# Optimization experiments

Hardware: AMD Instinct MI355X
Metric: run time of the kernel (lower is better)

## Reference

```python
import jax, jax.numpy as jnp
from jax import lax
import numpy as np

B, C, H, W = 32, 64, 80, 80


def setup_inputs() -> dict:
    key = jax.random.key(0)
    ks = jax.random.split(key, 9)
    x = jax.random.normal(ks[0], (B, C, H, W), dtype=jnp.float32)
    # gammas are zero-init Parameters in torch; use small random values so the
    # recurrence is non-trivial but numerically stable (spectral radius ~0.4).
    g = lambda k: jax.random.normal(k, (C, C), dtype=jnp.float32) * 0.05
    return {"x": x,
            "g1": g(ks[1]), "g2": g(ks[2]),
            "g4": g(ks[3]), "g5": g(ks[4]),
            "g7": g(ks[5]), "g8": g(ks[6]),
            "g10": g(ks[7]), "g11": g(ks[8])}


def _scan_dir(xh, gv, gh, apply_relu):
    """Row-major DAG recurrence over xh: [H, W, C, B].
    h[i,j] = act(x[i,j] + gv @ h[i-1,j] + gh @ h[i,j-1]).
    Zero carry at boundaries exactly reproduces the i>0 / j>0 guards
    (gamma @ 0 == 0)."""
    def row_step(prev_row, x_row):
        # prev_row: [W, C, B] -- vertical contribution for the whole row at once
        up = jnp.einsum('cd,wdb->wcb', gv, prev_row)
        def col_step(left, inp):
            xc, upc = inp                      # [C, B] each
            h = xc + upc + gh @ left
            if apply_relu:
                h = jax.nn.relu(h)
            return h, h
        _, row = lax.scan(col_step, jnp.zeros_like(x_row[0]), (x_row, up))
        return row, row
    _, out = lax.scan(row_step, jnp.zeros_like(xh[0]), xh)
    return out


def reference(x, g1, g2, g4, g5, g7, g8, g10, g11):
    # torch permutes to [C, B, H, W]; we use [H, W, C, B] so scans run over
    # leading axes and each cell is the same [C, B] matrix as hse[:, :, i, j].
    xh = jnp.transpose(x, (2, 3, 1, 0))  # [H, W, C, B]
    # SE: i forward, j forward, ReLU
    hse = _scan_dir(xh, g1, g2, True)
    # NE: i reversed, j forward, ReLU -> flip H
    hne = _scan_dir(xh[::-1], g4, g5, True)[::-1]
    # NW: i reversed, j reversed, ReLU -> flip H and W
    hnw = _scan_dir(xh[::-1, ::-1], g7, g8, True)[::-1, ::-1]
    # SW: i forward, j reversed, NO ReLU (omitted in the original code) -> flip W
    hsw = _scan_dir(xh[:, ::-1], g10, g11, False)[:, ::-1]
    out = hse + hne + hnw + hsw
    return jnp.transpose(out, (3, 2, 0, 1))  # back to [B, C, H, W]
```

## Files before the change

kernel.cpp:

```cpp
#include <hip/hip_runtime.h>
#include <stdint.h>

#define HH 80
#define WW 80
#define CC 64
#define BB 32
#define NDIAG (HH + WW - 1)
#define SLICE (HH * WW * CC)
#define NCW 5
#define NTHREADS 512

typedef _Float16 f16;
typedef _Float16 f16x8 __attribute__((ext_vector_type(8)));
typedef _Float16 f16x4 __attribute__((ext_vector_type(4)));
typedef float floatx4 __attribute__((ext_vector_type(4)));

struct GPtrs { const float* p[8]; };

__global__ __launch_bounds__(256) void xpose_kernel(const float* __restrict__ x,
                                                    f16* __restrict__ xT) {
  const int bi = blockIdx.x;
  const int b = bi / HH, i = bi - b * HH;
  __shared__ float tile[WW][CC + 1];
  const float* xp = x + ((size_t)(b * CC) * HH + i) * WW;
  for (int idx = threadIdx.x; idx < CC * WW; idx += 256) {
    const int c = idx / WW, j = idx - c * WW;
    tile[j][c] = xp[(size_t)c * (HH * WW) + j];
  }
  __syncthreads();
  f16* op = xT + (size_t)(b * HH + i) * WW * CC;
  for (int idx = threadIdx.x; idx < (WW * CC) / 4; idx += 256) {
    const int j = idx >> 4, m = idx & 15;
    f16x4 v;
    v[0] = (f16)tile[j][m * 4 + 0];
    v[1] = (f16)tile[j][m * 4 + 1];
    v[2] = (f16)tile[j][m * 4 + 2];
    v[3] = (f16)tile[j][m * 4 + 3];
    *(f16x4*)(op + j * CC + m * 4) = v;
  }
}

__global__ __launch_bounds__(NTHREADS, 1) void dag_kernel(const f16* __restrict__ xT,
                                                          GPtrs g,
                                                          f16* __restrict__ scratch) {
  const int blk = blockIdx.x;
  const int dir = blk >> 5;
  const int b   = blk & 31;
  const int tid = threadIdx.x;
  const int wv   = tid >> 6;
  const int lane = tid & 63;
  const int l15  = lane & 15;
  const int quad = lane >> 4;

  const bool fi      = (dir == 1) || (dir == 2);
  const bool fj      = (dir == 2) || (dir == 3);
  const bool do_relu = (dir != 3);
  const float* __restrict__ gv = g.p[2 * dir];
  const float* __restrict__ gh = g.p[2 * dir + 1];

  __align__(16) __shared__ f16 hbuf[2][HH + 2][CC + 8];
  __align__(16) __shared__ f16 xring[2][HH][CC + 8];

  for (int idx = tid; idx < 2 * (HH + 2) * (CC + 8); idx += NTHREADS)
    (&hbuf[0][0][0])[idx] = (f16)0.0f;

  const f16* const xTb = xT + (size_t)b * SLICE;
  f16* const sbase = scratch + (size_t)blk * SLICE;

  auto cellOff = [&](int dd, int cell) -> int {
    const int lo = max(0, dd - (WW - 1));
    const int hi = min(dd, HH - 1);
    const int ipc = min(max(cell, lo), hi);
    const int jp = dd - ipc;
    const int io1 = fi ? (HH - 1 - ipc) : ipc;
    const int jo1 = fj ? (WW - 1 - jp) : jp;
    return io1 * WW + jo1;
  };

  f16x8 Av[4][2], Ah[4][2];
  f16x8 xb[4];
  int ucell[4];
  const int cq = quad * 4;
  const int cm = lane >> 3;
  const int c8 = (lane & 7) * 8;

  if (wv < NCW) {
#pragma unroll
    for (int cb = 0; cb < 4; ++cb) {
      const int row = cb * 16 + l15;
      const float* pv = gv + row * CC;
      const float* ph = gh + row * CC;
#pragma unroll
      for (int jj = 0; jj < 8; ++jj) {
        Av[cb][0][jj] = (f16)pv[quad * 8 + jj];
        Av[cb][1][jj] = (f16)pv[32 + quad * 8 + jj];
        Ah[cb][0][jj] = (f16)ph[quad * 8 + jj];
        Ah[cb][1][jj] = (f16)ph[32 + quad * 8 + jj];
      }
    }
  } else {
    const int wio = wv - NCW;
#pragma unroll
    for (int k = 0; k < 4; ++k) ucell[k] = min(wio + 3 * k, 9) * 8 + cm;
    f16x8 b0[4];
#pragma unroll
    for (int k = 0; k < 4; ++k)
      b0[k] = *(const f16x8*)(xTb + (cellOff(0, ucell[k]) << 6) + c8);
#pragma unroll
    for (int k = 0; k < 4; ++k)
      *(f16x8*)&xring[0][ucell[k]][c8] = b0[k];
#pragma unroll
    for (int k = 0; k < 4; ++k)
      xb[k] = *(const f16x8*)(xTb + (cellOff(1, ucell[k]) << 6) + c8);
  }

  __syncthreads();

  for (int d = 0; d < NDIAG; ++d) {
    const int p = d & 1, q = p ^ 1;
    const int ilo = max(0, d - (WW - 1));
    const int ihi = min(d, HH - 1);

    if (wv < NCW) {
      const int ntiles = ((ihi - ilo) >> 4) + 1;
      if (wv < ntiles) {
        const int ip  = ilo + wv * 16 + l15;
        const int ipx = min(ip, ihi);
        const int su  = min(ip, HH + 1);
        const int sl  = min(ip + 1, HH + 1);
        const f16x8 bu0 = *(const f16x8*)&hbuf[q][su][quad * 8];
        const f16x8 bu1 = *(const f16x8*)&hbuf[q][su][32 + quad * 8];
        const f16x8 bl0 = *(const f16x8*)&hbuf[q][sl][quad * 8];
        const f16x8 bl1 = *(const f16x8*)&hbuf[q][sl][32 + quad * 8];
        const bool ok = (ip <= ihi);
#pragma unroll
        for (int cb = 0; cb < 4; ++cb) {
          const f16x4 xv = *(const f16x4*)&xring[p][ipx][cb * 16 + cq];
          floatx4 a;
          a[0] = (float)xv[0]; a[1] = (float)xv[1];
          a[2] = (float)xv[2]; a[3] = (float)xv[3];
          a = __builtin_amdgcn_mfma_f32_16x16x32_f16(Av[cb][0], bu0, a, 0, 0, 0);
          a = __builtin_amdgcn_mfma_f32_16x16x32_f16(Av[cb][1], bu1, a, 0, 0, 0);
          a = __builtin_amdgcn_mfma_f32_16x16x32_f16(Ah[cb][0], bl0, a, 0, 0, 0);
          a = __builtin_amdgcn_mfma_f32_16x16x32_f16(Ah[cb][1], bl1, a, 0, 0, 0);
          float h0 = a[0], h1 = a[1], h2 = a[2], h3 = a[3];
          if (do_relu) {
            h0 = fmaxf(h0, 0.f); h1 = fmaxf(h1, 0.f);
            h2 = fmaxf(h2, 0.f); h3 = fmaxf(h3, 0.f);
          }
          f16x4 hw;
          hw[0] = (f16)h0; hw[1] = (f16)h1; hw[2] = (f16)h2; hw[3] = (f16)h3;
          if (ok) *(f16x4*)&hbuf[p][ip + 1][cb * 16 + cq] = hw;
        }
      }
    } else {
      f16x8 nb[4];
      const int dpre = min(d + 2, NDIAG - 1);
#pragma unroll
      for (int k = 0; k < 4; ++k)
        nb[k] = *(const f16x8*)(xTb + (cellOff(dpre, ucell[k]) << 6) + c8);
      const int s1 = (d + 1) & 1;
#pragma unroll
      for (int k = 0; k < 4; ++k)
        *(f16x8*)&xring[s1][ucell[k]][c8] = xb[k];
      if (d >= 1) {
        const int dF = d - 1;
        const int lo = max(0, dF - (WW - 1)), hi = min(dF, HH - 1);
#pragma unroll
        for (int k = 0; k < 4; ++k) {
          const int ipc = min(max(ucell[k], lo), hi);
          const f16x8 hv = *(const f16x8*)&hbuf[q][ipc + 1][c8];
          *(f16x8*)(sbase + (cellOff(dF, ucell[k]) << 6) + c8) = hv;
        }
      }
#pragma unroll
      for (int k = 0; k < 4; ++k) xb[k] = nb[k];
    }

    __builtin_amdgcn_s_waitcnt(0xC07F);
    __builtin_amdgcn_s_barrier();
  }

  if (wv >= NCW) {
    const int dF = NDIAG - 1;
    const int lo = max(0, dF - (WW - 1)), hi = min(dF, HH - 1);
#pragma unroll
    for (int k = 0; k < 4; ++k) {
      const int ipc = min(max(ucell[k], lo), hi);
      const f16x8 hv = *(const f16x8*)&hbuf[dF & 1][ipc + 1][c8];
      *(f16x8*)(sbase + (cellOff(dF, ucell[k]) << 6) + c8) = hv;
    }
  }
}

__global__ __launch_bounds__(256) void reduce_kernel(const f16* __restrict__ s,
                                                     float* __restrict__ out) {
  const int bi = blockIdx.x;
  const int b = bi / HH, i = bi - b * HH;
  __shared__ float tile[WW][CC + 1];
  const size_t dstride = (size_t)BB * SLICE;
  const f16* p = s + (size_t)b * SLICE + (size_t)i * (WW * CC);
  for (int idx = threadIdx.x; idx < (WW * CC) / 8; idx += 256) {
    const int j = idx >> 3, c8 = (idx & 7) * 8;
    const size_t off = (size_t)j * CC + c8;
    const f16x8 a0 = *(const f16x8*)(p + off);
    const f16x8 a1 = *(const f16x8*)(p + off + dstride);
    const f16x8 a2 = *(const f16x8*)(p + off + 2 * dstride);
    const f16x8 a3 = *(const f16x8*)(p + off + 3 * dstride);
#pragma unroll
    for (int k = 0; k < 8; ++k)
      tile[j][c8 + k] = (float)a0[k] + (float)a1[k] + (float)a2[k] + (float)a3[k];
  }
  __syncthreads();
  float* op = out + ((size_t)(b * CC) * HH + i) * WW;
  const int c  = threadIdx.x >> 2;
  const int jb = (threadIdx.x & 3) * 4;
#pragma unroll
  for (int k = 0; k < 5; ++k) {
    const int j0 = jb + k * 16;
    floatx4 v;
    v[0] = tile[j0 + 0][c];
    v[1] = tile[j0 + 1][c];
    v[2] = tile[j0 + 2][c];
    v[3] = tile[j0 + 3][c];
    *(floatx4*)(op + (size_t)c * (HH * WW) + j0) = v;
  }
}

extern "C" void kernel_launch(void* const* d_in, const int* in_sizes, int n_in,
                              void* d_out, int out_size, void* d_ws, size_t ws_size,
                              hipStream_t stream) {
  const float* x = (const float*)d_in[0];
  GPtrs g;
  for (int k = 0; k < 8; ++k) g.p[k] = (const float*)d_in[k + 1];
  f16* xT = (f16*)d_ws;
  f16* scratch = xT + (size_t)BB * SLICE;

  xpose_kernel<<<BB * HH, 256, 0, stream>>>(x, xT);
  dag_kernel<<<4 * BB, NTHREADS, 0, stream>>>((const f16*)xT, g, scratch);
  reduce_kernel<<<BB * HH, 256, 0, stream>>>((const f16*)scratch, (float*)d_out);
}
```

Before: 252.4 us.

## Process two anti-diagonals per barrier with overlapping wave tiles

The DAG wavefront loop now advances two anti-diagonals per block barrier instead of one. Six compute waves each own a 16-row tile with stride 15, so a wave can finish the second diagonal from its own first-diagonal results without waiting on the others. Compute waves now prefetch their own x inputs straight from global memory into registers, which removes the shared-memory x ring. The two remaining waves flush two diagonals per step from a 4-slot h buffer. The aim is to halve the number of barriers, at the cost of redundant overlapping rows and more complex indexing.

```diff
diff --git a/kernel.cpp b/kernel.cpp
--- a/kernel.cpp
+++ b/kernel.cpp
@@ -6,8 +6,10 @@
 #define CC 64
 #define BB 32
 #define NDIAG (HH + WW - 1)
+#define NINT ((NDIAG + 1) / 2)
 #define SLICE (HH * WW * CC)
-#define NCW 5
+#define NCW 6
+#define STRIDE 15
 #define NTHREADS 512
 
 typedef _Float16 f16;
@@ -51,6 +53,7 @@
   const int lane = tid & 63;
   const int l15  = lane & 15;
   const int quad = lane >> 4;
+  const int cq   = quad * 4;
 
   const bool fi      = (dir == 1) || (dir == 2);
   const bool fj      = (dir == 2) || (dir == 3);
@@ -58,139 +61,130 @@
   const float* __restrict__ gv = g.p[2 * dir];
   const float* __restrict__ gh = g.p[2 * dir + 1];
 
-  __align__(16) __shared__ f16 hbuf[2][HH + 2][CC + 8];
-  __align__(16) __shared__ f16 xring[2][HH][CC + 8];
-
-  for (int idx = tid; idx < 2 * (HH + 2) * (CC + 8); idx += NTHREADS)
+  __align__(16) __shared__ f16 hbuf[4][HH + 2][CC + 8];
+  for (int idx = tid; idx < 4 * (HH + 2) * (CC + 8); idx += NTHREADS)
     (&hbuf[0][0][0])[idx] = (f16)0.0f;
+
+  f16x8 Av[4][2], Ah[4][2];
+#pragma unroll
+  for (int cb = 0; cb < 4; ++cb) {
+    const int row = cb * 16 + l15;
+    const float* pv = gv + row * CC;
+    const float* ph = gh + row * CC;
+#pragma unroll
+    for (int jj = 0; jj < 8; ++jj) {
+      Av[cb][0][jj] = (f16)pv[quad * 8 + jj];
+      Av[cb][1][jj] = (f16)pv[32 + quad * 8 + jj];
+      Ah[cb][0][jj] = (f16)ph[quad * 8 + jj];
+      Ah[cb][1][jj] = (f16)ph[32 + quad * 8 + jj];
+    }
+  }
 
   const f16* const xTb = xT + (size_t)b * SLICE;
   f16* const sbase = scratch + (size_t)blk * SLICE;
 
-  auto cellOff = [&](int dd, int cell) -> int {
+  auto xoff = [&](int dd, int r) -> int {
     const int lo = max(0, dd - (WW - 1));
     const int hi = min(dd, HH - 1);
-    const int ipc = min(max(cell, lo), hi);
-    const int jp = dd - ipc;
-    const int io1 = fi ? (HH - 1 - ipc) : ipc;
+    const int rc = min(max(r, lo), hi);
+    const int jp = dd - rc;
+    const int io1 = fi ? (HH - 1 - rc) : rc;
     const int jo1 = fj ? (WW - 1 - jp) : jp;
     return io1 * WW + jo1;
   };
 
-  f16x8 Av[4][2], Ah[4][2];
-  f16x8 xb[4];
-  int ucell[4];
-  const int cq = quad * 4;
-  const int cm = lane >> 3;
-  const int c8 = (lane & 7) * 8;
-
-  if (wv < NCW) {
+  auto pfetch = [&](int e1, f16x4 (*xv)[4]) {
+    const int d0 = 2 * e1;
+    const int d1c = min(2 * e1 + 1, NDIAG - 1);
+    const int aw = max(0, 2 * e1 + 1 - (HH - 1)) + STRIDE * wv;
+    const f16* p0 = xTb + xoff(d0, aw - 1 + l15) * CC + cq;
+#pragma unroll
+    for (int cb = 0; cb < 4; ++cb) xv[0][cb] = *(const f16x4*)(p0 + cb * 16);
+    const f16* p1 = xTb + xoff(d1c, aw + l15) * CC + cq;
+#pragma unroll
+    for (int cb = 0; cb < 4; ++cb) xv[1][cb] = *(const f16x4*)(p1 + cb * 16);
+  };
+
+  auto doTile = [&](int sR, int sW, int base, int lo, int hi,
+                    const f16x4* xv, bool cut15) {
+    const int ip = base + l15;
+    const int su = min(max(ip, 0), HH + 1);
+    const int sl = min(ip + 1, HH + 1);
+    const f16x8 bu0 = *(const f16x8*)&hbuf[sR][su][quad * 8];
+    const f16x8 bu1 = *(const f16x8*)&hbuf[sR][su][32 + quad * 8];
+    const f16x8 bl0 = *(const f16x8*)&hbuf[sR][sl][quad * 8];
+    const f16x8 bl1 = *(const f16x8*)&hbuf[sR][sl][32 + quad * 8];
+    const bool ok = (ip >= lo) && (ip <= hi) && (!cut15 || l15 < 15);
 #pragma unroll
     for (int cb = 0; cb < 4; ++cb) {
-      const int row = cb * 16 + l15;
-      const float* pv = gv + row * CC;
-      const float* ph = gh + row * CC;
-#pragma unroll
-      for (int jj = 0; jj < 8; ++jj) {
-        Av[cb][0][jj] = (f16)pv[quad * 8 + jj];
-        Av[cb][1][jj] = (f16)pv[32 + quad * 8 + jj];
-        Ah[cb][0][jj] = (f16)ph[quad * 8 + jj];
-        Ah[cb][1][jj] = (f16)ph[32 + quad * 8 + jj];
+      floatx4 a;
+      a[0] = (float)xv[cb][0]; a[1] = (float)xv[cb][1];
+      a[2] = (float)xv[cb][2]; a[3] = (float)xv[cb][3];
+      a = __builtin_amdgcn_mfma_f32_16x16x32_f16(Av[cb][0], bu0, a, 0, 0, 0);
+      a = __builtin_amdgcn_mfma_f32_16x16x32_f16(Av[cb][1], bu1, a, 0, 0, 0);
+      a = __builtin_amdgcn_mfma_f32_16x16x32_f16(Ah[cb][0], bl0, a, 0, 0, 0);
+      a = __builtin_amdgcn_mfma_f32_16x16x32_f16(Ah[cb][1], bl1, a, 0, 0, 0);
+      float h0 = a[0], h1 = a[1], h2 = a[2], h3 = a[3];
+      if (do_relu) {
+        h0 = fmaxf(h0, 0.f); h1 = fmaxf(h1, 0.f);
+        h2 = fmaxf(h2, 0.f); h3 = fmaxf(h3, 0.f);
       }
-    }
-  } else {
+      f16x4 hw;
+      hw[0] = (f16)h0; hw[1] = (f16)h1; hw[2] = (f16)h2; hw[3] = (f16)h3;
+      if (ok) *(f16x4*)&hbuf[sW][ip + 1][cb * 16 + cq] = hw;
+    }
+  };
+
+  const int c8io = (lane & 7) * 8;
+  auto flushDiag = [&](int dF) {
+    const int lo = max(0, dF - (WW - 1)), hi = min(dF, HH - 1);
     const int wio = wv - NCW;
 #pragma unroll
-    for (int k = 0; k < 4; ++k) ucell[k] = min(wio + 3 * k, 9) * 8 + cm;
-    f16x8 b0[4];
-#pragma unroll
-    for (int k = 0; k < 4; ++k)
-      b0[k] = *(const f16x8*)(xTb + (cellOff(0, ucell[k]) << 6) + c8);
-#pragma unroll
-    for (int k = 0; k < 4; ++k)
-      *(f16x8*)&xring[0][ucell[k]][c8] = b0[k];
-#pragma unroll
-    for (int k = 0; k < 4; ++k)
-      xb[k] = *(const f16x8*)(xTb + (cellOff(1, ucell[k]) << 6) + c8);
-  }
+    for (int k = 0; k < 5; ++k) {
+      const int cell = ((k * 2 + wio) << 3) + (lane >> 3);
+      if (cell >= lo && cell <= hi) {
+        const f16x8 hv = *(const f16x8*)&hbuf[dF & 3][cell + 1][c8io];
+        const int jp = dF - cell;
+        const int io1 = fi ? (HH - 1 - cell) : cell;
+        const int jo1 = fj ? (WW - 1 - jp) : jp;
+        *(f16x8*)(sbase + (io1 * WW + jo1) * CC + c8io) = hv;
+      }
+    }
+  };
+
+  f16x4 xc[2][4], xn[2][4];
+  if (wv < NCW) pfetch(0, xc);
 
   __syncthreads();
 
-  for (int d = 0; d < NDIAG; ++d) {
-    const int p = d & 1, q = p ^ 1;
-    const int ilo = max(0, d - (WW - 1));
-    const int ihi = min(d, HH - 1);
+  for (int e = 0; e < NINT; ++e) {
+    const int D0 = 2 * e, D1 = 2 * e + 1;
+    const int ilo0 = max(0, D0 - (WW - 1)), ihi0 = min(D0, HH - 1);
+    const int ilo1 = max(0, D1 - (WW - 1)), ihi1 = min(D1, HH - 1);
+    const int sm1 = (D0 - 1) & 3, s0 = D0 & 3, s1 = D1 & 3;
 
     if (wv < NCW) {
-      const int ntiles = ((ihi - ilo) >> 4) + 1;
-      if (wv < ntiles) {
-        const int ip  = ilo + wv * 16 + l15;
-        const int ipx = min(ip, ihi);
-        const int su  = min(ip, HH + 1);
-        const int sl  = min(ip + 1, HH + 1);
-        const f16x8 bu0 = *(const f16x8*)&hbuf[q][su][quad * 8];
-        const f16x8 bu1 = *(const f16x8*)&hbuf[q][su][32 + quad * 8];
-        const f16x8 bl0 = *(const f16x8*)&hbuf[q][sl][quad * 8];
-        const f16x8 bl1 = *(const f16x8*)&hbuf[q][sl][32 + quad * 8];
-        const bool ok = (ip <= ihi);
-#pragma unroll
-        for (int cb = 0; cb < 4; ++cb) {
-          const f16x4 xv = *(const f16x4*)&xring[p][ipx][cb * 16 + cq];
-          floatx4 a;
-          a[0] = (float)xv[0]; a[1] = (float)xv[1];
-          a[2] = (float)xv[2]; a[3] = (float)xv[3];
-          a = __builtin_amdgcn_mfma_f32_16x16x32_f16(Av[cb][0], bu0, a, 0, 0, 0);
-          a = __builtin_amdgcn_mfma_f32_16x16x32_f16(Av[cb][1], bu1, a, 0, 0, 0);
-          a = __builtin_amdgcn_mfma_f32_16x16x32_f16(Ah[cb][0], bl0, a, 0, 0, 0);
-          a = __builtin_amdgcn_mfma_f32_16x16x32_f16(Ah[cb][1], bl1, a, 0, 0, 0);
-          float h0 = a[0], h1 = a[1], h2 = a[2], h3 = a[3];
-          if (do_relu) {
-            h0 = fmaxf(h0, 0.f); h1 = fmaxf(h1, 0.f);
-            h2 = fmaxf(h2, 0.f); h3 = fmaxf(h3, 0.f);
-          }
-          f16x4 hw;
-          hw[0] = (f16)h0; hw[1] = (f16)h1; hw[2] = (f16)h2; hw[3] = (f16)h3;
-          if (ok) *(f16x4*)&hbuf[p][ip + 1][cb * 16 + cq] = hw;
-        }
+      pfetch(min(e + 1, NINT - 1), xn);
+      const int aw = ilo1 + STRIDE * wv;
+      if ((aw - 1 <= ihi0) || (aw <= ihi1)) {
+        doTile(sm1, s0, aw - 1, ilo0, ihi0, xc[0], false);
+        __builtin_amdgcn_s_waitcnt(0xC07F);
+        doTile(s0, s1, aw, ilo1, ihi1, xc[1], true);
       }
+#pragma unroll
+      for (int t = 0; t < 2; ++t)
+#pragma unroll
+        for (int cb = 0; cb < 4; ++cb) xc[t][cb] = xn[t][cb];
     } else {
-      f16x8 nb[4];
-      const int dpre = min(d + 2, NDIAG - 1);
-#pragma unroll
-      for (int k = 0; k < 4; ++k)
-        nb[k] = *(const f16x8*)(xTb + (cellOff(dpre, ucell[k]) << 6) + c8);
-      const int s1 = (d + 1) & 1;
-#pragma unroll
-      for (int k = 0; k < 4; ++k)
-        *(f16x8*)&xring[s1][ucell[k]][c8] = xb[k];
-      if (d >= 1) {
-        const int dF = d - 1;
-        const int lo = max(0, dF - (WW - 1)), hi = min(dF, HH - 1);
-#pragma unroll
-        for (int k = 0; k < 4; ++k) {
-          const int ipc = min(max(ucell[k], lo), hi);
-          const f16x8 hv = *(const f16x8*)&hbuf[q][ipc + 1][c8];
-          *(f16x8*)(sbase + (cellOff(dF, ucell[k]) << 6) + c8) = hv;
-        }
-      }
-#pragma unroll
-      for (int k = 0; k < 4; ++k) xb[k] = nb[k];
+      if (D0 >= 2) flushDiag(D0 - 2);
+      if (D0 >= 1) flushDiag(D0 - 1);
     }
 
     __builtin_amdgcn_s_waitcnt(0xC07F);
     __builtin_amdgcn_s_barrier();
   }
 
-  if (wv >= NCW) {
-    const int dF = NDIAG - 1;
-    const int lo = max(0, dF - (WW - 1)), hi = min(dF, HH - 1);
-#pragma unroll
-    for (int k = 0; k < 4; ++k) {
-      const int ipc = min(max(ucell[k], lo), hi);
-      const f16x8 hv = *(const f16x8*)&hbuf[dF & 1][ipc + 1][c8];
-      *(f16x8*)(sbase + (cellOff(dF, ucell[k]) << 6) + c8) = hv;
-    }
-  }
+  if (wv >= NCW) flushDiag(NDIAG - 1);
 }
 
 __global__ __launch_bounds__(256) void reduce_kernel(const f16* __restrict__ s,
```

New measurement: 260.9 us. 3.4% more time.
